# Kernel optimization log

Hardware: AMD Instinct MI355X
Metric: run time of the kernel (lower is better)

## Reference

```python
import jax, jax.numpy as jnp
import numpy as np

TOP_K = 4
NEG_N = 5
NEG_SEED = 1234  # fixed seed replacing python random.sample for determinism


def setup_inputs() -> dict:
    key = jax.random.key(0)
    k1, k2, k3 = jax.random.split(key, 3)
    B, D, R, S = 16, 256, 1024, 20
    vit_feature = jax.random.normal(k1, (B, D, R), dtype=jnp.float32)
    lag_feature = jax.random.normal(k2, (B, S, D), dtype=jnp.float32)
    lag_vit_map = jax.random.normal(k3, (B, S, R), dtype=jnp.float32)
    return {"vit_feature": vit_feature, "lag_feature": lag_feature,
            "lag_vit_map": lag_vit_map}


def reference(vit_feature, lag_feature, lag_vit_map):
    # permutes from the original torch code
    m = jnp.transpose(lag_vit_map, (0, 2, 1))    # (B, R, S)
    vit = jnp.transpose(vit_feature, (0, 2, 1))  # (B, R, D)
    lag_tok = lag_feature                        # (B, S, D): token kk's feature is lag[b][:, kk] after permute == lag_feature[b, kk, :]
    B, R, D = vit.shape

    # topk language tokens per visual row
    _, cols = jax.lax.top_k(m, TOP_K)            # (B, R, TOP_K) int32 indices into S

    # vit_corrspondence_feature[jj] = stack_b vit[b, jj, :]  -> (R, B, D)
    vit_corr = jnp.transpose(vit, (1, 0, 2))

    # lag_corrspondence_feature[jj][b] = stack_k lag_tok[b, cols[b,jj,k], :] -> (R, B, K, D)
    gather_tok = jax.vmap(lambda t, c: t[c])     # t:(S,D), c:(R,K) -> (R,K,D)
    lag_corr = jnp.transpose(gather_tok(lag_tok, cols), (1, 0, 2, 3))

    # negatives: original code's inner loop only keeps the LAST batch index (B-1).
    # It samples NEG_N rows without replacement from range(R), excluding jj when
    # that index equals ii (here ii == B-1 for the surviving sample is only
    # relevant when the outer ii == B-1; exclusion is applied on the diagonal).
    skey = jax.random.key(NEG_SEED)
    scores = jax.random.uniform(skey, (R, B, R))          # random scores for sampling w/o replacement
    rr = jnp.arange(R)
    scores = scores.at[rr, B - 1, rr].set(-1.0)           # exclude jj for ii == B-1
    _, neg_idx = jax.lax.top_k(scores, NEG_N)             # (R, B, NEG_N)
    neg = vit[B - 1][neg_idx]                             # (R, B, NEG_N, D)

    return vit_corr, lag_corr, neg
```

## Files before the change

### kernel.cpp

```cpp
#include <hip/hip_runtime.h>
#include <stdint.h>

#define R_DIM 1024
#define B_DIM 16
#define D_DIM 256
#define S_DIM 20

typedef float f32x4 __attribute__((ext_vector_type(4)));

__device__ __forceinline__ void threefry2x32_1234(uint32_t x0, uint32_t x1,
                                                  uint32_t& o0, uint32_t& o1) {
  const uint32_t ks1 = 1234u;
  const uint32_t ks2 = 1234u ^ 0x1BD11BDAu;
  x1 += ks1;
#define TF_ROUND(r) { x0 += x1; x1 = (x1 << (r)) | (x1 >> (32 - (r))); x1 ^= x0; }
  TF_ROUND(13) TF_ROUND(15) TF_ROUND(26) TF_ROUND(6)
  x0 += ks1; x1 += ks2 + 1u;
  TF_ROUND(17) TF_ROUND(29) TF_ROUND(16) TF_ROUND(24)
  x0 += ks2; x1 += 2u;
  TF_ROUND(13) TF_ROUND(15) TF_ROUND(26) TF_ROUND(6)
  x1 += ks1 + 3u;
  TF_ROUND(17) TF_ROUND(29) TF_ROUND(16) TF_ROUND(24)
  x0 += ks1; x1 += ks2 + 4u;
  TF_ROUND(13) TF_ROUND(15) TF_ROUND(26) TF_ROUND(6)
  x0 += ks2; x1 += 5u;
#undef TF_ROUND
  o0 = x0; o1 = x1;
}

__device__ __forceinline__ unsigned long long wave_max_u64(unsigned long long v) {
#pragma unroll
  for (int off = 1; off < 64; off <<= 1) {
    unsigned long long o = __shfl_xor(v, off, 64);
    v = (o > v) ? o : v;
  }
  return v;
}

__global__ __launch_bounds__(256) void kA(const float* __restrict__ vit,
                                          const float* __restrict__ lag_feature,
                                          const float* __restrict__ lag_vit_map,
                                          float* __restrict__ out0,
                                          float* __restrict__ out1) {
  if (blockIdx.x < 4096) {
    __shared__ float tile[32][33];
    const int id = blockIdx.x;
    const int bx = id & 31;
    const int by = (id >> 5) & 7;
    const int bz = id >> 8;
    const int r0 = bx * 32, d0 = by * 32;
    const int tx = threadIdx.x & 31, ty = threadIdx.x >> 5;
    const float* src = vit + (size_t)bz * D_DIM * R_DIM;
#pragma unroll
    for (int i = 0; i < 4; ++i) {
      int d = d0 + ty + i * 8;
      tile[ty + i * 8][tx] = src[(size_t)d * R_DIM + r0 + tx];
    }
    __syncthreads();
    if (bz == 15) {
#pragma unroll
      for (int i = 0; i < 4; ++i) {
        int r = r0 + ty + i * 8;
        out0[((size_t)r * B_DIM + bz) * D_DIM + d0 + tx] = tile[tx][ty + i * 8];
      }
    } else {
#pragma unroll
      for (int i = 0; i < 4; ++i) {
        int r = r0 + ty + i * 8;
        __builtin_nontemporal_store(tile[tx][ty + i * 8],
                                    &out0[((size_t)r * B_DIM + bz) * D_DIM + d0 + tx]);
      }
    }
  } else {
    const int tid = (blockIdx.x - 4096) * 256 + threadIdx.x;
    const int lane = threadIdx.x & 63;
    const int row = tid >> 6;
    const int r = row >> 4;
    const int b = row & 15;

    unsigned long long key = 0ull;
    if (lane < S_DIM) {
      float f = lag_vit_map[((size_t)b * S_DIM + lane) * R_DIM + r];
      uint32_t u = __float_as_uint(f);
      uint32_t ok = u ^ (uint32_t)(((int32_t)u >> 31) | 0x80000000u);
      key = ((unsigned long long)ok << 32) | (0xFFFFFFFFu - (uint32_t)lane);
    }

    uint32_t cols[4];
#pragma unroll
    for (int k = 0; k < 4; ++k) {
      unsigned long long m = wave_max_u64(key);
      cols[k] = 0xFFFFFFFFu - (uint32_t)m;
      if (key == m) key = 0ull;
    }

#pragma unroll
    for (int k = 0; k < 4; ++k) {
      const f32x4* src = (const f32x4*)(lag_feature + ((size_t)b * S_DIM + cols[k]) * D_DIM);
      f32x4* dst = (f32x4*)(out1 + ((size_t)row * 4 + k) * D_DIM);
      __builtin_nontemporal_store(src[lane], &dst[lane]);
    }
  }
}

__device__ __forceinline__ void top5_mask(unsigned long long* keys, uint32_t* idx) {
#pragma unroll
  for (int n = 0; n < 5; ++n) {
    unsigned long long lm = keys[0];
#pragma unroll
    for (int t = 1; t < 16; ++t) lm = (keys[t] > lm) ? keys[t] : lm;
    unsigned long long g = wave_max_u64(lm);
    idx[n] = 0xFFFFFFFFu - (uint32_t)g;
#pragma unroll
    for (int t = 0; t < 16; ++t)
      if (keys[t] == g) keys[t] = 0ull;
  }
}

__global__ __launch_bounds__(256) void kB(const float* __restrict__ out0,
                                          float* __restrict__ out2) {
  const int tid = blockIdx.x * blockDim.x + threadIdx.x;
  const int lane = threadIdx.x & 63;
  const int row = tid >> 6;
  const int r = row >> 4, b = row & 15;

  unsigned long long keys[16];
  const uint32_t base = (uint32_t)row * 1024u;
#pragma unroll
  for (int t = 0; t < 16; ++t) {
    uint32_t s = (uint32_t)lane + ((uint32_t)t << 6);
    uint32_t o0, o1;
    threefry2x32_1234(0u, base + s, o0, o1);
    uint32_t bits = o0 ^ o1;
    unsigned long long k =
        ((unsigned long long)(bits >> 9) << 32) | (0xFFFFFFFFu - s);
    if (b == 15 && s == (uint32_t)r) k = 0ull;
    keys[t] = k;
  }

  uint32_t idx[5];
  top5_mask(keys, idx);

#pragma unroll
  for (int n = 0; n < 5; ++n) {
    const f32x4* src = (const f32x4*)(out0 + ((size_t)idx[n] * B_DIM + 15) * D_DIM);
    f32x4* dst = (f32x4*)(out2 + ((size_t)row * 5 + n) * D_DIM);
    __builtin_nontemporal_store(src[lane], &dst[lane]);
  }
}

extern "C" void kernel_launch(void* const* d_in, const int* in_sizes, int n_in,
                              void* d_out, int out_size, void* d_ws, size_t ws_size,
                              hipStream_t stream) {
  (void)in_sizes; (void)n_in; (void)d_ws; (void)ws_size; (void)out_size;
  const float* vit = (const float*)d_in[0];
  const float* lag = (const float*)d_in[1];
  const float* map = (const float*)d_in[2];
  float* out = (float*)d_out;
  float* out0 = out;
  float* out1 = out + 4194304;
  float* out2 = out + 4194304 + 16777216;

  kA<<<8192, 256, 0, stream>>>(vit, lag, map, out0, out1);
  kB<<<4096, 256, 0, stream>>>(out0, out2);
}
```

Before: 218.3 us.

## Interleave transpose, topk-gather and negative-sampling roles in one kernel

A small pre-kernel transposes only batch 15 of vit into a workspace buffer. A single main kernel then interleaves three block roles (negative sampling with threefry top-5, vit transpose, top-4 lag gather) by blockIdx modulo 3, instead of running negative sampling in a separate second kernel. The aim is to overlap the compute-heavy RNG work with the memory-bound copies and to drop the dependency on out0. The cost is an extra small launch, the workspace traffic, and mixed register pressure across roles within one kernel.

```diff
diff --git a/kernel.cpp b/kernel.cpp
--- a/kernel.cpp
+++ b/kernel.cpp
@@ -37,52 +37,111 @@
   return v;
 }
 
-__global__ __launch_bounds__(256) void kA(const float* __restrict__ vit,
-                                          const float* __restrict__ lag_feature,
-                                          const float* __restrict__ lag_vit_map,
-                                          float* __restrict__ out0,
-                                          float* __restrict__ out1) {
-  if (blockIdx.x < 4096) {
+__device__ __forceinline__ void top5_mask(unsigned long long* keys, uint32_t* idx) {
+#pragma unroll
+  for (int n = 0; n < 5; ++n) {
+    unsigned long long lm = keys[0];
+#pragma unroll
+    for (int t = 1; t < 16; ++t) lm = (keys[t] > lm) ? keys[t] : lm;
+    unsigned long long g = wave_max_u64(lm);
+    idx[n] = 0xFFFFFFFFu - (uint32_t)g;
+#pragma unroll
+    for (int t = 0; t < 16; ++t)
+      if (keys[t] == g) keys[t] = 0ull;
+  }
+}
+
+__global__ __launch_bounds__(256) void kT(const float* __restrict__ vit,
+                                          float* __restrict__ vit15T) {
+  __shared__ float tile[32][33];
+  const int bx = blockIdx.x & 31;
+  const int by = blockIdx.x >> 5;
+  const int r0 = bx * 32, d0 = by * 32;
+  const int tx = threadIdx.x & 31, ty = threadIdx.x >> 5;
+  const float* src = vit + (size_t)15 * D_DIM * R_DIM;
+#pragma unroll
+  for (int i = 0; i < 4; ++i) {
+    int d = d0 + ty + i * 8;
+    tile[ty + i * 8][tx] = src[(size_t)d * R_DIM + r0 + tx];
+  }
+  __syncthreads();
+#pragma unroll
+  for (int i = 0; i < 4; ++i) {
+    int r = r0 + ty + i * 8;
+    vit15T[(size_t)r * D_DIM + d0 + tx] = tile[tx][ty + i * 8];
+  }
+}
+
+__global__ __launch_bounds__(256) void kMain(const float* __restrict__ vit,
+                                             const float* __restrict__ lag_feature,
+                                             const float* __restrict__ lag_vit_map,
+                                             const float* __restrict__ vit15T,
+                                             float* __restrict__ out0,
+                                             float* __restrict__ out1,
+                                             float* __restrict__ out2) {
+  const int role = blockIdx.x % 3;
+  const int u = blockIdx.x / 3;
+  const int lane = threadIdx.x & 63;
+  const int wv = threadIdx.x >> 6;
+
+  if (role == 0) {
+    const int row = u * 4 + wv;
+    const int r = row >> 4, b = row & 15;
+
+    unsigned long long keys[16];
+    const uint32_t base = (uint32_t)row * 1024u;
+#pragma unroll
+    for (int t = 0; t < 16; ++t) {
+      uint32_t s = (uint32_t)lane + ((uint32_t)t << 6);
+      uint32_t o0, o1;
+      threefry2x32_1234(0u, base + s, o0, o1);
+      uint32_t bits = o0 ^ o1;
+      unsigned long long k =
+          ((unsigned long long)(bits >> 9) << 32) | (0xFFFFFFFFu - s);
+      if (b == 15 && s == (uint32_t)r) k = 0ull;
+      keys[t] = k;
+    }
+
+    uint32_t idx[5];
+    top5_mask(keys, idx);
+
+#pragma unroll
+    for (int n = 0; n < 5; ++n) {
+      const f32x4* src = (const f32x4*)(vit15T + (size_t)idx[n] * D_DIM);
+      f32x4* dst = (f32x4*)(out2 + ((size_t)row * 5 + n) * D_DIM);
+      __builtin_nontemporal_store(src[lane], &dst[lane]);
+    }
+  } else if (role == 1) {
     __shared__ float tile[32][33];
-    const int id = blockIdx.x;
-    const int bx = id & 31;
-    const int by = (id >> 5) & 7;
-    const int bz = id >> 8;
+    const int b = u >> 8;
+    const int t8 = u & 255;
+    const int bx = t8 & 31;
+    const int by = t8 >> 5;
     const int r0 = bx * 32, d0 = by * 32;
     const int tx = threadIdx.x & 31, ty = threadIdx.x >> 5;
-    const float* src = vit + (size_t)bz * D_DIM * R_DIM;
+    const float* src = vit + (size_t)b * D_DIM * R_DIM;
 #pragma unroll
     for (int i = 0; i < 4; ++i) {
       int d = d0 + ty + i * 8;
       tile[ty + i * 8][tx] = src[(size_t)d * R_DIM + r0 + tx];
     }
     __syncthreads();
-    if (bz == 15) {
 #pragma unroll
-      for (int i = 0; i < 4; ++i) {
-        int r = r0 + ty + i * 8;
-        out0[((size_t)r * B_DIM + bz) * D_DIM + d0 + tx] = tile[tx][ty + i * 8];
-      }
-    } else {
-#pragma unroll
-      for (int i = 0; i < 4; ++i) {
-        int r = r0 + ty + i * 8;
-        __builtin_nontemporal_store(tile[tx][ty + i * 8],
-                                    &out0[((size_t)r * B_DIM + bz) * D_DIM + d0 + tx]);
-      }
+    for (int i = 0; i < 4; ++i) {
+      int r = r0 + ty + i * 8;
+      __builtin_nontemporal_store(tile[tx][ty + i * 8],
+                                  &out0[((size_t)r * B_DIM + b) * D_DIM + d0 + tx]);
     }
   } else {
-    const int tid = (blockIdx.x - 4096) * 256 + threadIdx.x;
-    const int lane = threadIdx.x & 63;
-    const int row = tid >> 6;
+    const int row = u * 4 + wv;
     const int r = row >> 4;
     const int b = row & 15;
 
     unsigned long long key = 0ull;
     if (lane < S_DIM) {
       float f = lag_vit_map[((size_t)b * S_DIM + lane) * R_DIM + r];
-      uint32_t u = __float_as_uint(f);
-      uint32_t ok = u ^ (uint32_t)(((int32_t)u >> 31) | 0x80000000u);
+      uint32_t uu = __float_as_uint(f);
+      uint32_t ok = uu ^ (uint32_t)(((int32_t)uu >> 31) | 0x80000000u);
       key = ((unsigned long long)ok << 32) | (0xFFFFFFFFu - (uint32_t)lane);
     }
 
@@ -103,56 +162,10 @@
   }
 }
 
-__device__ __forceinline__ void top5_mask(unsigned long long* keys, uint32_t* idx) {
-#pragma unroll
-  for (int n = 0; n < 5; ++n) {
-    unsigned long long lm = keys[0];
-#pragma unroll
-    for (int t = 1; t < 16; ++t) lm = (keys[t] > lm) ? keys[t] : lm;
-    unsigned long long g = wave_max_u64(lm);
-    idx[n] = 0xFFFFFFFFu - (uint32_t)g;
-#pragma unroll
-    for (int t = 0; t < 16; ++t)
-      if (keys[t] == g) keys[t] = 0ull;
-  }
-}
-
-__global__ __launch_bounds__(256) void kB(const float* __restrict__ out0,
-                                          float* __restrict__ out2) {
-  const int tid = blockIdx.x * blockDim.x + threadIdx.x;
-  const int lane = threadIdx.x & 63;
-  const int row = tid >> 6;
-  const int r = row >> 4, b = row & 15;
-
-  unsigned long long keys[16];
-  const uint32_t base = (uint32_t)row * 1024u;
-#pragma unroll
-  for (int t = 0; t < 16; ++t) {
-    uint32_t s = (uint32_t)lane + ((uint32_t)t << 6);
-    uint32_t o0, o1;
-    threefry2x32_1234(0u, base + s, o0, o1);
-    uint32_t bits = o0 ^ o1;
-    unsigned long long k =
-        ((unsigned long long)(bits >> 9) << 32) | (0xFFFFFFFFu - s);
-    if (b == 15 && s == (uint32_t)r) k = 0ull;
-    keys[t] = k;
-  }
-
-  uint32_t idx[5];
-  top5_mask(keys, idx);
-
-#pragma unroll
-  for (int n = 0; n < 5; ++n) {
-    const f32x4* src = (const f32x4*)(out0 + ((size_t)idx[n] * B_DIM + 15) * D_DIM);
-    f32x4* dst = (f32x4*)(out2 + ((size_t)row * 5 + n) * D_DIM);
-    __builtin_nontemporal_store(src[lane], &dst[lane]);
-  }
-}
-
 extern "C" void kernel_launch(void* const* d_in, const int* in_sizes, int n_in,
                               void* d_out, int out_size, void* d_ws, size_t ws_size,
                               hipStream_t stream) {
-  (void)in_sizes; (void)n_in; (void)d_ws; (void)ws_size; (void)out_size;
+  (void)in_sizes; (void)n_in; (void)ws_size; (void)out_size;
   const float* vit = (const float*)d_in[0];
   const float* lag = (const float*)d_in[1];
   const float* map = (const float*)d_in[2];
@@ -160,7 +173,8 @@
   float* out0 = out;
   float* out1 = out + 4194304;
   float* out2 = out + 4194304 + 16777216;
+  float* vit15T = (float*)d_ws;
 
-  kA<<<8192, 256, 0, stream>>>(vit, lag, map, out0, out1);
-  kB<<<4096, 256, 0, stream>>>(out0, out2);
+  kT<<<256, 256, 0, stream>>>(vit, vit15T);
+  kMain<<<12288, 256, 0, stream>>>(vit, lag, map, vit15T, out0, out1, out2);
 }
```

Result: faster. 212.8 us (-2.5%).
